# Kernel optimization log

Measured on AMD Instinct MI355X. Metric: run time of the kernel, lower is better.

Reference implementation:

```python
import jax, jax.numpy as jnp
import numpy as np

# Loihi neuron constants (from init params: iDecay=1024, vDecay=128, vThMant=80, wgtExp=0)
I_DECAY = 1024.0
V_DECAY = 128.0
THETA = 80.0 * 64.0       # vThMant << 6
W_SCALE = 64.0            # 1 << (6 + wgtExp)


def _trunc_decay(s, decay):
    # Loihi fixed-point decay: trunc(s * (4096 - decay) / 4096)
    smooth = s * ((4096.0 - decay) / 4096.0)
    return smooth + jax.lax.stop_gradient(jnp.trunc(smooth) - smooth)


def _loihi(x):
    # x: [N, C, T] weighted spikes -> binary spikes [N, C, T]
    zero = jnp.zeros(x.shape[:-1], x.dtype)

    def step(carry, xt):
        u, v = carry
        u = _trunc_decay(u, I_DECAY) + W_SCALE * xt
        v = _trunc_decay(v, V_DECAY) + u
        spike = (v >= THETA).astype(v.dtype)
        v = v * (1.0 - spike)  # reset on spike (refDelay=1)
        return (u, v), spike

    _, s = jax.lax.scan(step, (zero, zero), jnp.moveaxis(x, -1, 0))
    return jnp.moveaxis(s, 0, -1)


def _delay_shift(x):
    # shift spike train by one time step along last axis
    return jnp.pad(x, ((0, 0), (0, 0), (1, 0)))[..., :-1]


def setup_inputs() -> dict:
    key = jax.random.key(0)
    k = jax.random.split(key, 5)
    N, T = 32, 400
    spike_rate = 0.1
    tact = (jax.random.uniform(k[0], (N, 156, T)) < spike_rate).astype(jnp.float32)
    vis = (jax.random.uniform(k[1], (N, 6300, T)) < spike_rate).astype(jnp.float32)
    W_tact = 0.1 * jax.random.normal(k[2], (512, 156), jnp.float32)
    W_vis = 0.1 * jax.random.normal(k[3], (512, 6300), jnp.float32)
    W_combi = 0.1 * jax.random.normal(k[4], (256, 1024), jnp.float32)
    return {"spikeInputTact": tact, "spikeInputVis": vis,
            "W_tact": W_tact, "W_vis": W_vis, "W_combi": W_combi}


def reference(spikeInputTact, spikeInputVis, W_tact, W_vis, W_combi):
    # dense = per-time-step linear: [o,i] x [n,i,t] -> [n,o,t]
    tact = _delay_shift(_loihi(jnp.einsum('oi,nit->not', W_tact, spikeInputTact)))
    vis = _delay_shift(_loihi(jnp.einsum('oi,nit->not', W_vis, spikeInputVis)))
    combi = jnp.concatenate([tact, vis], axis=1)  # [N, 1024, T]
    out = _delay_shift(_loihi(jnp.einsum('oi,nit->not', W_combi, combi)))
    return out
```

## Files before the change

kernel.cpp:

```cpp
#include <hip/hip_runtime.h>


typedef unsigned short u16;
typedef unsigned int u32;
typedef __attribute__((ext_vector_type(4))) short short4v;
typedef __attribute__((ext_vector_type(8))) short short8;
typedef __attribute__((ext_vector_type(4))) float f32x4;

#define GLOAD16(g, l)                                                         \
    __builtin_amdgcn_global_load_lds(                                         \
        (const __attribute__((address_space(1))) u32*)(g),                    \
        (__attribute__((address_space(3))) u32*)(l), 16, 0, 0)

__device__ __forceinline__ u16 f2bf_trunc(float x) {
    return (u16)(__float_as_uint(x) >> 16);
}

__device__ __forceinline__ void cvt_wide(const float* __restrict__ S,
                                         u16* __restrict__ Sp,
                                         int I, int KLD, int n, int i0, int t0,
                                         u16 (*tile)[268])
{
    const int tid = threadIdx.x;
    const int il = tid >> 2;
    const int q  = tid & 3;

    #pragma unroll
    for (int ii = 0; ii < 4; ++ii) {
        const int gi = i0 + ii * 64 + il;
        const bool iok = gi < I;
        const float* srow = S + ((size_t)n * I + gi) * 400 + t0;
        #pragma unroll
        for (int s = 0; s < 4; ++s) {
            const int tl = (s * 4 + q) * 4;
            float4 v = make_float4(0.f, 0.f, 0.f, 0.f);
            if (iok && (t0 + tl) < 400)
                v = *(const float4*)(srow + tl);
            tile[tl + 0][ii * 64 + il] = f2bf_trunc(v.x);
            tile[tl + 1][ii * 64 + il] = f2bf_trunc(v.y);
            tile[tl + 2][ii * 64 + il] = f2bf_trunc(v.z);
            tile[tl + 3][ii * 64 + il] = f2bf_trunc(v.w);
        }
    }
    __syncthreads();

    const int row = tid >> 3;
    const int lc  = tid & 7;
    #pragma unroll
    for (int h = 0; h < 2; ++h) {
        const int tl = h * 32 + row;
        const int t = t0 + tl;
        if (t < 400) {
            u16* dst = Sp + (size_t)(n * 400 + t) * KLD + i0;
            #pragma unroll
            for (int w = 0; w < 4; ++w) {
                const int io = w * 64 + lc * 8;
                *(short4v*)(dst + io)     = *(const short4v*)&tile[tl][io];
                *(short4v*)(dst + io + 4) = *(const short4v*)&tile[tl][io + 4];
            }
        }
    }
    __syncthreads();
}

__device__ __forceinline__ void cvt_body(const float* __restrict__ S,
                                         u16* __restrict__ Sp,
                                         int I, int KLD, int n, int i0, int t0,
                                         u16 (*tile)[88])
{
    const int tid = threadIdx.x;
    const int il = tid >> 2;
    const int q  = tid & 3;
    const int gi = i0 + il;
    const bool iok = gi < I;
    const float* srow = S + ((size_t)n * I + gi) * 400 + t0;

    #pragma unroll
    for (int s = 0; s < 4; ++s) {
        const int tl = (s * 4 + q) * 4;
        float4 v = make_float4(0.f, 0.f, 0.f, 0.f);
        if (iok && (t0 + tl) < 400)
            v = *(const float4*)(srow + tl);
        tile[tl + 0][il] = f2bf_trunc(v.x);
        tile[tl + 1][il] = f2bf_trunc(v.y);
        tile[tl + 2][il] = f2bf_trunc(v.z);
        tile[tl + 3][il] = f2bf_trunc(v.w);
    }
    __syncthreads();

    const int tl = tid >> 2;
    const int iq = tid & 3;
    const int t  = t0 + tl;
    const int go = i0 + iq * 16;
    if (t < 400 && go < KLD) {
        u16* dst = Sp + (size_t)(n * 400 + t) * KLD + go;
        *(short8*)(dst)     = *(const short8*)&tile[tl][iq * 16];
        *(short8*)(dst + 8) = *(const short8*)&tile[tl][iq * 16 + 8];
    }
    __syncthreads();
}

__device__ __forceinline__ void split_one(const float* __restrict__ W,
                                          u16* __restrict__ W2,
                                          int C, int K, int KLD, int idx)
{
    const int c = idx / KLD;
    const int k = idx - c * KLD;
    float w = (k < K) ? W[(size_t)c * K + k] : 0.f;
    u32 b  = __float_as_uint(w);
    u32 hb = (b + 0x7FFFu + ((b >> 16) & 1u)) & 0xFFFF0000u;
    float r = w - __uint_as_float(hb);
    u32 rb = __float_as_uint(r);
    u32 mb = (rb + 0x7FFFu + ((rb >> 16) & 1u)) & 0xFFFF0000u;
    const int rh = ((c >> 4) << 5) | (c & 15);
    W2[(size_t)rh * KLD + k]        = (u16)(hb >> 16);
    W2[(size_t)(rh + 16) * KLD + k] = (u16)(mb >> 16);
}

__global__ __launch_bounds__(256) void prep(
    const float* __restrict__ vis, const float* __restrict__ tact,
    const float* __restrict__ Wv, const float* __restrict__ Wt,
    const float* __restrict__ Wc,
    u16* __restrict__ Sv, u16* __restrict__ St,
    u16* __restrict__ Wv2, u16* __restrict__ Wt2, u16* __restrict__ Wc2)
{
    __shared__ u16 tile[64][268];
    const int b = blockIdx.x;
    if (b < 5600) {
        const int x = b % 7, y = (b / 7) % 25, n = b / 175;
        cvt_wide(vis, Sv, 6300, 6400, n, y * 256, x * 64, tile);
    } else if (b < 6496) {
        const int b2 = b - 5600;
        const int x = b2 % 7, y = (b2 / 7) % 4, n = b2 / 28;
        cvt_body(tact, St, 156, 256, n, y * 64, x * 64, (u16(*)[88])tile);
    } else {
        const int b3 = b - 6496;
        for (int e = b3 * 256 + (int)threadIdx.x; e < 3670016; e += 1024 * 256) {
            if (e < 3276800)        split_one(Wv, Wv2, 512, 6300, 6400, e);
            else if (e < 3407872)   split_one(Wt, Wt2, 512, 156,  256,  e - 3276800);
            else                    split_one(Wc, Wc2, 256, 1024, 1024, e - 3407872);
        }
    }
}

__device__ __forceinline__ void gemm_core(
    const u16* __restrict__ A, const u16* __restrict__ B,
    float* __restrict__ X, int M2, int KLD, int kt0, int nk,
    int bx, int by, u16* lds)
{
    const int c0  = bx * 256;
    const int nt0 = by * 256;
    const int tid  = threadIdx.x;
    const int lane = tid & 63, w = tid >> 6;
    const int wm = w >> 2, wn = w & 3;
    const int l15 = lane & 15, l16 = lane >> 4;

    const int swzg  = (l16 ^ ((l15 >> 1) & 3)) * 8;
    const int aBase = (wm * 128 + l15) * 32 + swzg;
    const int bBase = 16384 + (wn * 64 + l15) * 32 + swzg;

    const int gsw = ((tid & 3) ^ ((tid >> 3) & 3)) * 8;
    const u16* pA = A + (size_t)(c0 + (tid >> 2)) * KLD + gsw;
    const u16* pB = B + (size_t)(nt0 + (tid >> 2)) * KLD + gsw;
    u16* const ldsW = &lds[w * 512];

#define STG(op, d, ks, tt) do {                                               \
    const u16* s_ = ((op) ? pB : pA) + (size_t)(tt) * 64 + (ks) * 32;         \
    GLOAD16(s_, ldsW + (d) * 32768 + (op) * 16384 + (ks) * 8192);             \
    GLOAD16(s_ + (size_t)128 * KLD,                                           \
            ldsW + (d) * 32768 + (op) * 16384 + (ks) * 8192 + 4096);          \
} while (0)

#define PH(d, ks, mh, LOADB, STAGE_STMT, WAIT_STMT) do {                      \
    short8 a_[4];                                                             \
    _Pragma("unroll")                                                         \
    for (int mf = 0; mf < 4; ++mf)                                            \
        a_[mf] = *(const short8*)&lds[(d) * 32768 + (ks) * 8192 + aBase       \
                                      + ((mh) * 4 + mf) * 512];               \
    if (LOADB) {                                                              \
        _Pragma("unroll")                                                     \
        for (int nf = 0; nf < 4; ++nf)                                        \
            bcur[nf] = *(const short8*)&lds[(d) * 32768 + (ks) * 8192 + bBase \
                                            + nf * 512];                      \
    }                                                                         \
    STAGE_STMT;                                                               \
    __builtin_amdgcn_s_barrier();                                             \
    asm volatile("s_waitcnt lgkmcnt(0)" ::: "memory");                        \
    __builtin_amdgcn_sched_barrier(0);                                        \
    __builtin_amdgcn_s_setprio(1);                                            \
    _Pragma("unroll")                                                         \
    for (int mf = 0; mf < 4; ++mf)                                            \
        _Pragma("unroll")                                                     \
        for (int nf = 0; nf < 4; ++nf)                                        \
            acc[(mh) * 4 + mf][nf] = __builtin_amdgcn_mfma_f32_16x16x32_bf16( \
                a_[mf], bcur[nf], acc[(mh) * 4 + mf][nf], 0, 0, 0);           \
    __builtin_amdgcn_s_setprio(0);                                            \
    WAIT_STMT;                                                                \
    __builtin_amdgcn_s_barrier();                                             \
    asm volatile("" ::: "memory");                                            \
} while (0)

    f32x4 acc[8][4];
    #pragma unroll
    for (int i = 0; i < 8; ++i)
        #pragma unroll
        for (int j = 0; j < 4; ++j)
            acc[i][j] = (f32x4){0.f, 0.f, 0.f, 0.f};

    STG(0, 0, 0, kt0); STG(1, 0, 0, kt0); STG(0, 0, 1, kt0); STG(1, 0, 1, kt0);
    STG(0, 1, 0, kt0 + 1); STG(1, 1, 0, kt0 + 1); STG(1, 1, 1, kt0 + 1);
    asm volatile("s_waitcnt vmcnt(0)" ::: "memory");
    __builtin_amdgcn_s_barrier();
    asm volatile("" ::: "memory");

    const int I = nk >> 1;
    for (int i = 0; i < I; ++i) {
        const int t = kt0 + 2 * i;
        const bool pf = (i < I - 1);
        short8 bcur[4];
        PH(0, 0, 0, 1, { STG(0, 1, 1, t + 1); }, );
        PH(0, 0, 1, 0, { if (pf) STG(1, 0, 0, t + 2); }, );
        PH(0, 1, 0, 1, { if (pf) STG(0, 0, 0, t + 2); }, );
        PH(0, 1, 1, 0, { if (pf) STG(1, 0, 1, t + 2); },
           { if (pf) asm volatile("s_waitcnt vmcnt(6)" ::: "memory");
             else    asm volatile("s_waitcnt vmcnt(0)" ::: "memory"); });
        PH(1, 0, 0, 1, { if (pf) STG(0, 0, 1, t + 2); }, );
        PH(1, 0, 1, 0, { if (pf) STG(1, 1, 0, t + 3); }, );
        PH(1, 1, 0, 1, { if (pf) STG(0, 1, 0, t + 3); }, );
        PH(1, 1, 1, 0, { if (pf) STG(1, 1, 1, t + 3); },
           { if (pf) asm volatile("s_waitcnt vmcnt(6)" ::: "memory");
             else    asm volatile("s_waitcnt vmcnt(0)" ::: "memory"); });
    }

    const int Mout = M2 >> 1;
    #pragma unroll
    for (int j = 0; j < 4; ++j) {
        const int cg = bx * 128 + wm * 64 + j * 16 + l16 * 4;
        #pragma unroll
        for (int nf = 0; nf < 4; ++nf) {
            const int nt = nt0 + wn * 64 + nf * 16 + l15;
            f32x4 s = acc[2 * j][nf] + acc[2 * j + 1][nf];
            *(f32x4*)&X[(size_t)nt * Mout + cg] = s;
        }
    }
#undef STG
#undef PH
}

__global__ __launch_bounds__(512, 2) void gemm_l1(
    const u16* __restrict__ Av, const u16* __restrict__ Bv, float* __restrict__ Xv,
    const u16* __restrict__ At, const u16* __restrict__ Bt, float* __restrict__ Xt)
{
    __shared__ u16 lds[65536];
    const int f = blockIdx.x + 4 * (blockIdx.y + 50 * blockIdx.z);
    if (f < 200) {
        int bx, by;
        if (f < 192) {
            const int m = f >> 4, r = f & 15;
            by = m * 4 + ((r & 7) >> 1);
            bx = ((r >> 3) << 1) | (r & 1);
        } else {
            const int k = f - 192;
            by = 48 + (k >> 2);
            bx = k & 3;
        }
        gemm_core(Av, Bv, Xv, 1024, 6400, 0, 100, bx, by, lds);
    } else {
        const int f2 = f - 200;
        gemm_core(At, Bt, Xt, 1024, 256, 0, 4, f2 & 3, f2 >> 2, lds);
    }
}

__global__ __launch_bounds__(512, 2) void gemm_g(
    const u16* __restrict__ A, const u16* __restrict__ B,
    float* __restrict__ Xbase, int M2, int KLD, int ktPerZ)
{
    __shared__ u16 lds[65536];
    const int Dx = gridDim.x, Dy = gridDim.y;
    int f = blockIdx.x + Dx * (blockIdx.y + Dy * blockIdx.z);
    const int nwg = Dx * Dy * gridDim.z;
    f = (f & 7) * (nwg >> 3) + (f >> 3);
    const int bx = f % Dx;
    const int by = (f / Dx) % Dy;
    const int bz = f / (Dx * Dy);
    gemm_core(A, B, Xbase + (size_t)bz * 12800 * (M2 >> 1), M2, KLD,
              bz * ktPerZ, ktPerZ, bx, by, lds);
}

__device__ __forceinline__ float loihi_step(float xt, float& u, float& v)
{
    u = truncf(u * 0.75f) + 64.f * xt;
    v = truncf(v * 0.96875f) + u;
    if (v >= 5120.f) { v = 0.f; return 1.f; }
    return 0.f;
}

__global__ __launch_bounds__(64) void scan_ab(const float* __restrict__ Xt,
                                              const float* __restrict__ Xv,
                                              u16* __restrict__ Sc)
{
    const int gid = blockIdx.x * 64 + threadIdx.x;
    const int n = gid >> 10;
    const int c = gid & 1023;
    const float* xr = (c < 512)
        ? Xt + (size_t)(n * 400) * 512 + c
        : Xv + (size_t)(n * 400) * 512 + (c - 512);
    u16* srow = Sc + (size_t)(n * 400) * 1024 + c;
    srow[0] = 0;

    float c0[8], c1[8], c2[8];
    #pragma unroll
    for (int d = 0; d < 8; ++d) c0[d] = xr[(size_t)d * 512];
    #pragma unroll
    for (int d = 0; d < 8; ++d) c1[d] = xr[(size_t)(8 + d) * 512];

    float u = 0.f, v = 0.f;
    for (int blk = 0; blk < 50; ++blk) {
        const int tb = blk * 8;
        #pragma unroll
        for (int d = 0; d < 8; ++d) {
            const int tl = tb + 16 + d;
            c2[d] = (tl < 400) ? xr[(size_t)tl * 512] : 0.f;
        }
        #pragma unroll
        for (int d = 0; d < 8; ++d) {
            const int t = tb + d;
            const float sp = loihi_step(c0[d], u, v);
            if (t < 399) srow[(size_t)(t + 1) * 1024] = (sp != 0.f) ? (u16)0x3F80 : (u16)0;
        }
        #pragma unroll
        for (int d = 0; d < 8; ++d) { c0[d] = c1[d]; c1[d] = c2[d]; }
    }
}

__global__ __launch_bounds__(64) void scan_c(const float* __restrict__ Xc,
                                             float* __restrict__ out)
{
    const int gid = blockIdx.x * 64 + threadIdx.x;
    const int n = gid >> 8;
    const int c = gid & 255;
    const size_t PS = (size_t)12800 * 256;
    const float* xr = Xc + (size_t)(n * 400) * 256 + c;
    float* orow = out + ((size_t)n * 256 + c) * 400;
    orow[0] = 0.f;

    float a0[8], b0[8], a1[8], b1[8], a2[8], b2[8];
    #pragma unroll
    for (int d = 0; d < 8; ++d) {
        a0[d] = xr[(size_t)d * 256];
        b0[d] = xr[(size_t)d * 256 + PS];
    }
    #pragma unroll
    for (int d = 0; d < 8; ++d) {
        a1[d] = xr[(size_t)(8 + d) * 256];
        b1[d] = xr[(size_t)(8 + d) * 256 + PS];
    }

    float u = 0.f, v = 0.f;
    for (int blk = 0; blk < 50; ++blk) {
        const int tb = blk * 8;
        #pragma unroll
        for (int d = 0; d < 8; ++d) {
            const int tl = tb + 16 + d;
            a2[d] = (tl < 400) ? xr[(size_t)tl * 256] : 0.f;
            b2[d] = (tl < 400) ? xr[(size_t)tl * 256 + PS] : 0.f;
        }
        #pragma unroll
        for (int d = 0; d < 8; ++d) {
            const int t = tb + d;
            const float sp = loihi_step(a0[d] + b0[d], u, v);
            if (t < 399) orow[t + 1] = sp;
        }
        #pragma unroll
        for (int d = 0; d < 8; ++d) {
            a0[d] = a1[d]; b0[d] = b1[d];
            a1[d] = a2[d]; b1[d] = b2[d];
        }
    }
}

extern "C" void kernel_launch(void* const* d_in, const int* in_sizes, int n_in,
                              void* d_out, int out_size, void* d_ws, size_t ws_size,
                              hipStream_t stream)
{
    const float* tact   = (const float*)d_in[0];
    const float* vis    = (const float*)d_in[1];
    const float* W_tact = (const float*)d_in[2];
    const float* W_vis  = (const float*)d_in[3];
    const float* W_comb = (const float*)d_in[4];
    float* out = (float*)d_out;

    const int NT = 32 * 400;
    const int Ktp = 256;
    const int Kvp = 6400;
    const int Kc  = 1024;

    char* p = (char*)d_ws;
    u16* Sv  = (u16*)p;                p += (size_t)NT * Kvp * 2;
    u16* St  = (u16*)p;                p += (size_t)NT * Ktp * 2;
    u16* Wt2 = (u16*)p;                p += (size_t)1024 * Ktp * 2;
    u16* Wv2 = (u16*)p;                p += (size_t)1024 * Kvp * 2;
    u16* Wc2 = (u16*)p;                p += (size_t)512 * Kc * 2;
    float* Xv = (float*)p;             p += (size_t)NT * 512 * 4;
    float* Xt = (float*)p;             p += (size_t)NT * 512 * 4;
    u16*   Sc = (u16*)Sv;
    float* Xc = (float*)((char*)Sv + (size_t)NT * 1024 * 2);

    prep<<<dim3(7520), 256, 0, stream>>>(vis, tact, W_vis, W_tact, W_comb,
                                         Sv, St, Wv2, Wt2, Wc2);

    gemm_l1<<<dim3(4, 50, 2), 512, 0, stream>>>(Wv2, Sv, Xv, Wt2, St, Xt);

    scan_ab<<<dim3((32 * 1024) / 64), 64, 0, stream>>>(Xt, Xv, Sc);

    gemm_g<<<dim3(2, 50, 2), 512, 0, stream>>>(Wc2, Sc, Xc, 512, Kc, 8);
    scan_c<<<dim3((32 * 256) / 64), 64, 0, stream>>>(Xc, out);

    (void)in_sizes; (void)n_in; (void)out_size; (void)ws_size;
}
```

Measured before the change: 354.9 us.

## Double-buffer A fragments in registers and move LDS staging after barrier

The GEMM main loop now prefetches the next phase's A fragments from LDS into a ping-pong register pair (aX/aY) while the current MFMAs run. The global-to-LDS stage and vmcnt wait move after the barrier, dropping one barrier and the lgkmcnt(0) wait per phase. The prologue and the order of tile stages are reshuffled to match the new dependency pattern. This aims to hide LDS read latency behind MFMA work, at the cost of more VGPRs and a more fragile ordering of stages and waits, with a risk of LDS races.

New measurement: 342.6 us. 1.04x faster.

```diff
diff --git a/kernel.cpp b/kernel.cpp
--- a/kernel.cpp
+++ b/kernel.cpp
@@ -171,21 +171,18 @@
             ldsW + (d) * 32768 + (op) * 16384 + (ks) * 8192 + 4096);          \
 } while (0)
 
-#define PH(d, ks, mh, LOADB, STAGE_STMT, WAIT_STMT) do {                      \
-    short8 a_[4];                                                             \
-    _Pragma("unroll")                                                         \
-    for (int mf = 0; mf < 4; ++mf)                                            \
-        a_[mf] = *(const short8*)&lds[(d) * 32768 + (ks) * 8192 + aBase       \
-                                      + ((mh) * 4 + mf) * 512];               \
+#define PH(d, ks, mh, LOADB, dn, ksn, mhn, AIN, AOUT, STAGE_STMT, WAIT_STMT)  \
+do {                                                                          \
     if (LOADB) {                                                              \
         _Pragma("unroll")                                                     \
         for (int nf = 0; nf < 4; ++nf)                                        \
             bcur[nf] = *(const short8*)&lds[(d) * 32768 + (ks) * 8192 + bBase \
                                             + nf * 512];                      \
     }                                                                         \
-    STAGE_STMT;                                                               \
-    __builtin_amdgcn_s_barrier();                                             \
-    asm volatile("s_waitcnt lgkmcnt(0)" ::: "memory");                        \
+    _Pragma("unroll")                                                         \
+    for (int mf = 0; mf < 4; ++mf)                                            \
+        AOUT[mf] = *(const short8*)&lds[(dn) * 32768 + (ksn) * 8192 + aBase   \
+                                        + ((mhn) * 4 + mf) * 512];            \
     __builtin_amdgcn_sched_barrier(0);                                        \
     __builtin_amdgcn_s_setprio(1);                                            \
     _Pragma("unroll")                                                         \
@@ -193,12 +190,17 @@
         _Pragma("unroll")                                                     \
         for (int nf = 0; nf < 4; ++nf)                                        \
             acc[(mh) * 4 + mf][nf] = __builtin_amdgcn_mfma_f32_16x16x32_bf16( \
-                a_[mf], bcur[nf], acc[(mh) * 4 + mf][nf], 0, 0, 0);           \
+                AIN[mf], bcur[nf], acc[(mh) * 4 + mf][nf], 0, 0, 0);          \
     __builtin_amdgcn_s_setprio(0);                                            \
-    WAIT_STMT;                                                                \
     __builtin_amdgcn_s_barrier();                                             \
     asm volatile("" ::: "memory");                                            \
+    STAGE_STMT;                                                               \
+    WAIT_STMT;                                                                \
+    asm volatile("" ::: "memory");                                            \
 } while (0)
+
+#define VM6 asm volatile("s_waitcnt vmcnt(6)" ::: "memory")
+#define VM0 asm volatile("s_waitcnt vmcnt(0)" ::: "memory")
 
     f32x4 acc[8][4];
     #pragma unroll
@@ -208,28 +210,32 @@
             acc[i][j] = (f32x4){0.f, 0.f, 0.f, 0.f};
 
     STG(0, 0, 0, kt0); STG(1, 0, 0, kt0); STG(0, 0, 1, kt0); STG(1, 0, 1, kt0);
-    STG(0, 1, 0, kt0 + 1); STG(1, 1, 0, kt0 + 1); STG(1, 1, 1, kt0 + 1);
-    asm volatile("s_waitcnt vmcnt(0)" ::: "memory");
+    STG(0, 1, 0, kt0 + 1); STG(1, 1, 0, kt0 + 1);
+    VM0;
     __builtin_amdgcn_s_barrier();
     asm volatile("" ::: "memory");
+
+    short8 aX[4], aY[4], bcur[4];
+    #pragma unroll
+    for (int mf = 0; mf < 4; ++mf)
+        aX[mf] = *(const short8*)&lds[aBase + mf * 512];
 
     const int I = nk >> 1;
     for (int i = 0; i < I; ++i) {
         const int t = kt0 + 2 * i;
         const bool pf = (i < I - 1);
-        short8 bcur[4];
-        PH(0, 0, 0, 1, { STG(0, 1, 1, t + 1); }, );
-        PH(0, 0, 1, 0, { if (pf) STG(1, 0, 0, t + 2); }, );
-        PH(0, 1, 0, 1, { if (pf) STG(0, 0, 0, t + 2); }, );
-        PH(0, 1, 1, 0, { if (pf) STG(1, 0, 1, t + 2); },
-           { if (pf) asm volatile("s_waitcnt vmcnt(6)" ::: "memory");
-             else    asm volatile("s_waitcnt vmcnt(0)" ::: "memory"); });
-        PH(1, 0, 0, 1, { if (pf) STG(0, 0, 1, t + 2); }, );
-        PH(1, 0, 1, 0, { if (pf) STG(1, 1, 0, t + 3); }, );
-        PH(1, 1, 0, 1, { if (pf) STG(0, 1, 0, t + 3); }, );
-        PH(1, 1, 1, 0, { if (pf) STG(1, 1, 1, t + 3); },
-           { if (pf) asm volatile("s_waitcnt vmcnt(6)" ::: "memory");
-             else    asm volatile("s_waitcnt vmcnt(0)" ::: "memory"); });
+        PH(0, 0, 0, 1, 0, 0, 1, aX, aY, { STG(1, 1, 1, t + 1); },
+           { if (pf) VM6; else VM0; });
+        PH(0, 0, 1, 0, 0, 1, 0, aY, aX, { STG(0, 1, 1, t + 1); }, );
+        PH(0, 1, 0, 1, 0, 1, 1, aX, aY, { if (pf) STG(1, 0, 0, t + 2); },
+           { if (pf) VM6; else VM0; });
+        PH(0, 1, 1, 0, 1, 0, 0, aY, aX, { if (pf) STG(0, 0, 0, t + 2); }, );
+        PH(1, 0, 0, 1, 1, 0, 1, aX, aY, { if (pf) STG(1, 0, 1, t + 2); },
+           { if (pf) VM6; else VM0; });
+        PH(1, 0, 1, 0, 1, 1, 0, aY, aX, { if (pf) STG(0, 0, 1, t + 2); }, );
+        PH(1, 1, 0, 1, 1, 1, 1, aX, aY, { if (pf) STG(1, 1, 0, t + 3); },
+           { if (pf) VM6; else VM0; });
+        PH(1, 1, 1, 0, 0, 0, 0, aY, aX, { if (pf) STG(0, 1, 0, t + 3); }, );
     }
 
     const int Mout = M2 >> 1;
@@ -245,6 +251,8 @@
     }
 #undef STG
 #undef PH
+#undef VM6
+#undef VM0
 }
 
 __global__ __launch_bounds__(512, 2) void gemm_l1(
```
